# Kernel optimization log

Hardware: AMD Instinct MI355X
Metric: run time of the kernel (lower is better)

## Reference

```python
import jax, jax.numpy as jnp
import numpy as np

WS = 4        # window_size
HEADS = 4     # num_heads
DIM = 128

def _rel_pos_idx(ws):
    # (ws*ws, ws*ws) int index into (2*ws-1)^2 bias table, as in Swin
    coords = np.stack(np.meshgrid(np.arange(ws), np.arange(ws), indexing='ij'))  # (2,ws,ws)
    cf = coords.reshape(2, -1)                       # (2, n)
    rel = cf[:, :, None] - cf[:, None, :]            # (2, n, n)
    rel = rel.transpose(1, 2, 0).astype(np.int64)    # (n, n, 2)
    rel[:, :, 0] += ws - 1
    rel[:, :, 1] += ws - 1
    rel[:, :, 0] *= 2 * ws - 1
    return jnp.asarray(rel.sum(-1))                  # (n, n)

def setup_inputs() -> dict:
    key = jax.random.key(0)
    ks = jax.random.split(key, 6)
    B, H, W, C = 16, 128, 128, DIM
    return {
        "x": jax.random.normal(ks[0], (B, H * W, C), dtype=jnp.float32),
        "H": H,
        "W": W,
        "qkv_w": jax.random.normal(ks[1], (C, 3 * C), dtype=jnp.float32) * 0.02,
        "qkv_b": jax.random.normal(ks[2], (3 * C,), dtype=jnp.float32) * 0.02,
        "proj_w": jax.random.normal(ks[3], (C, C), dtype=jnp.float32) * 0.02,
        "proj_b": jax.random.normal(ks[4], (C,), dtype=jnp.float32) * 0.02,
        "bias_tbl": jax.random.normal(ks[5], ((2 * WS - 1) ** 2, HEADS), dtype=jnp.float32) * 0.02,
    }

def reference(x, H, W, qkv_w, qkv_b, proj_w, proj_b, bias_tbl):
    B, N, C = x.shape
    hd = C // HEADS
    scale = hd ** -0.5
    n = WS * WS
    Hn, Wn = H // WS, W // WS
    # window partition: (B,N,C) -> (B*nW, ws*ws, C)
    xw = x.reshape(B, Hn, WS, Wn, WS, C).transpose(0, 1, 3, 2, 4, 5).reshape(-1, n, C)
    nW = xw.shape[0]
    qkv = xw @ qkv_w + qkv_b                               # (nW, n, 3C)
    qkv = qkv.reshape(nW, n, 3, HEADS, hd).transpose(2, 0, 3, 1, 4)
    q, k, v = qkv[0], qkv[1], qkv[2]                       # (nW, heads, n, hd)
    attn = jnp.einsum('whnd,whmd->whnm', q, k) * scale     # (nW, heads, n, n)
    idx = _rel_pos_idx(WS)
    bias = bias_tbl[idx.reshape(-1)].reshape(n, n, HEADS).transpose(2, 0, 1)  # (heads,n,n)
    attn = jax.nn.softmax(attn + bias[None], axis=-1)
    out = jnp.einsum('whnm,whmd->whnd', attn, v)           # (nW, heads, n, hd)
    out = out.transpose(0, 2, 1, 3).reshape(nW, n, C)
    out = out @ proj_w + proj_b
    # window reverse: (B*nW, n, C) -> (B, N, C)
    out = out.reshape(B, Hn, Wn, WS, WS, C).transpose(0, 1, 3, 2, 4, 5).reshape(B, N, C)
    return out
```

## Files before the change

kernel.cpp:

```cpp
#include <hip/hip_runtime.h>

typedef unsigned short u16;
typedef unsigned int   u32;
typedef __attribute__((ext_vector_type(8))) short bf16x8;
typedef __attribute__((ext_vector_type(4))) short bf16x4;
typedef __attribute__((ext_vector_type(4))) float f32x4;
typedef __attribute__((ext_vector_type(2))) u32 u32x2;

union F8 { bf16x8 v; u32 u[4]; };
union F4 { bf16x4 v; u32 u[2]; };

__device__ __forceinline__ u16 f2b(float f) {
    unsigned u = __builtin_bit_cast(unsigned, f);
    return (u16)((u + 0x7FFFu + ((u >> 16) & 1u)) >> 16);
}
__device__ __forceinline__ u32 pkbf(float a, float b) {
    return ((u32)f2b(b) << 16) | (u32)f2b(a);
}

__device__ __forceinline__ f32x4 mfma16(F4 a, F4 b, f32x4 c) {
    F8 a8, b8;
    a8.u[0] = a.u[0]; a8.u[1] = a.u[1]; a8.u[2] = 0; a8.u[3] = 0;
    b8.u[0] = b.u[0]; b8.u[1] = b.u[1]; b8.u[2] = 0; b8.u[3] = 0;
    return __builtin_amdgcn_mfma_f32_16x16x32_bf16(a8.v, b8.v, c, 0, 0, 0);
}

__device__ __forceinline__ void stage_tile(const u16* wfrag, u16* ldsbase,
                                           int t, int wave, int lane) {
    const char* gp = (const char*)wfrag + (((t * 4 + wave) << 10) | (lane << 4));
    char* lp = (char*)ldsbase + (((t % 3) << 12) | (wave << 10));
    __builtin_amdgcn_global_load_lds(
        (const __attribute__((address_space(1))) void*)gp,
        (__attribute__((address_space(3))) void*)lp, 16, 0, 0);
}

#define PIPE_WAIT(N) { asm volatile("s_waitcnt vmcnt(" #N ")" ::: "memory"); \
    __builtin_amdgcn_sched_barrier(0); __builtin_amdgcn_s_barrier(); }

__global__ void prep_kernel(const float* __restrict__ qkv_w,
                            const float* __restrict__ proj_w,
                            const float* __restrict__ bias_tbl,
                            const float* __restrict__ qkv_b,
                            u16* __restrict__ wsb, float* __restrict__ wsf)
{
    const float scale = 0.17677669529663689f;
    int tid = blockIdx.x * 256 + threadIdx.x;
    if (tid < 49152) {
        int i = tid & 7, l = (tid >> 3) & 63, w = (tid >> 9) & 3, t = tid >> 11;
        int nt;
        if (t < 16) { int h = t >> 2, r = t & 3;
                      nt = (r < 2) ? (2 * h + r) : (8 + 2 * h + (r - 2)); }
        else nt = t;
        int k = w * 32 + (l >> 4) * 8 + i;
        int col = nt * 16 + (l & 15);
        float wv = qkv_w[k * 384 + col];
        if (col < 128) wv *= scale;
        wsb[tid] = f2b(wv);
    } else if (tid < 57344) {
        int e = tid - 49152;
        int nt = e >> 10, rem = e & 1023;
        int c = rem >> 7, le = rem & 127, l = le >> 1, j = le & 1;
        int col = nt * 16 + (l & 15);
        int d = c * 16 + 4 * (l >> 4) + 2 * j;
        u32 val = ((u32)f2b(proj_w[(d + 1) * 128 + col]) << 16)
                |  (u32)f2b(proj_w[d * 128 + col]);
        ((u32*)wsb)[(24 + nt) * 1024 + c * 128 + l * 2 + j] = val;
    } else if (tid < 58368) {
        int e = tid - 57344;
        int h = e >> 8, t1 = (e >> 4) & 15, t2 = e & 15;
        int idx = ((t1 >> 2) - (t2 >> 2) + 3) * 7 + ((t1 & 3) - (t2 & 3) + 3);
        wsf[32768 + e] = bias_tbl[idx * 4 + h];
    } else if (tid < 58752) {
        int e = tid - 58368;
        wsf[33792 + e] = qkv_b[e] * (e < 128 ? scale : 1.0f);
    }
}

__global__ __launch_bounds__(256, 4) void winattn_kernel(
    const float* __restrict__ x, const u16* __restrict__ wfrag,
    const float* __restrict__ proj_b, float* __restrict__ out)
{
    __shared__ alignas(16) u16 lds[11776];
    u16* ring = lds;
    float* qkvbL  = (float*)(lds + 8704);
    float* biasL  = (float*)(lds + 9472);
    float* projbL = (float*)(lds + 11520);

    const int tid  = threadIdx.x;
    const int wave = tid >> 6, lane = tid & 63;
    const int g = lane >> 4, q16 = lane & 15;
    u16* scrA = lds + 6144 + wave * 640;
    u16* scrB = scrA + 320;

    const float* wsf = (const float*)wfrag;
    for (int e = tid; e < 384;  e += 256) qkvbL[e] = wsf[33792 + e];
    for (int e = tid; e < 1024; e += 256) biasL[e] = wsf[32768 + e];
    if (tid < 128) projbL[tid] = proj_b[tid];

    const int wpair = blockIdx.x * 4 + wave;
    const int wid0  = wpair * 2;
    const int b = wid0 >> 10, rem = wid0 & 1023, wi = rem >> 5, wj = rem & 31;
    const int nTok = (wi * 4 + (q16 >> 2)) * 128 + wj * 4 + (q16 & 3);
    const float* xrowA = x + ((long)b * 16384 + nTok) * 128;
    const float* xrowB = xrowA + 512;

    F8 axA[4], axB[4];
    #pragma unroll
    for (int ks = 0; ks < 4; ++ks) {
        const float4* pA = (const float4*)(xrowA + ks * 32 + g * 8);
        float4 a0 = pA[0], a1 = pA[1];
        axA[ks].u[0] = pkbf(a0.x, a0.y); axA[ks].u[1] = pkbf(a0.z, a0.w);
        axA[ks].u[2] = pkbf(a1.x, a1.y); axA[ks].u[3] = pkbf(a1.z, a1.w);
        const float4* pB = (const float4*)(xrowB + ks * 32 + g * 8);
        float4 b0 = pB[0], b1 = pB[1];
        axB[ks].u[0] = pkbf(b0.x, b0.y); axB[ks].u[1] = pkbf(b0.z, b0.w);
        axB[ks].u[2] = pkbf(b1.x, b1.y); axB[ks].u[3] = pkbf(b1.z, b1.w);
    }
    __builtin_amdgcn_sched_barrier(0);
    __syncthreads();

    stage_tile(wfrag, lds, 0, wave, lane);
    stage_tile(wfrag, lds, 1, wave, lane);

    f32x4 z4 = {0.f, 0.f, 0.f, 0.f};
    F4 ones; ones.u[0] = 0x3f803f80u; ones.u[1] = 0x3f803f80u;
    F4 pPA[4], pPB[4];
    float rsA4[4], rsB4[4];
    u32 OpkA[8][2], OpkB[8][2];

    #pragma unroll
    for (int h = 0; h < 4; ++h) {
        u32 QA[2][2], QB[2][2], KA[2][2], KB[2][2];
        #pragma unroll
        for (int r = 0; r < 4; ++r) {
            int t = 4 * h + r;
            PIPE_WAIT(1);
            const u16* slot = ring + (t % 3) * 2048;
            int nt = (r < 2) ? (2 * h + r) : (8 + 2 * h + (r - 2));
            float4 bb = *(const float4*)&qkvbL[nt * 16 + 4 * g];
            f32x4 accA = {bb.x, bb.y, bb.z, bb.w}, accB = accA;
            #pragma unroll
            for (int ks = 0; ks < 4; ++ks) {
                bf16x8 frag = *(const bf16x8*)(slot + ks * 512 + lane * 8);
                accA = __builtin_amdgcn_mfma_f32_16x16x32_bf16(frag, axA[ks].v, accA, 0, 0, 0);
                accB = __builtin_amdgcn_mfma_f32_16x16x32_bf16(frag, axB[ks].v, accB, 0, 0, 0);
            }
            u32 a0 = pkbf(accA[0], accA[1]), a1 = pkbf(accA[2], accA[3]);
            u32 b0 = pkbf(accB[0], accB[1]), b1 = pkbf(accB[2], accB[3]);
            if (r < 2) { QA[r][0] = a0; QA[r][1] = a1; QB[r][0] = b0; QB[r][1] = b1; }
            else { KA[r-2][0] = a0; KA[r-2][1] = a1; KB[r-2][0] = b0; KB[r-2][1] = b1; }
            stage_tile(wfrag, lds, t + 2, wave, lane);
        }
        F8 kfA, qfA, kfB, qfB;
        kfA.u[0]=KA[0][0]; kfA.u[1]=KA[0][1]; kfA.u[2]=KA[1][0]; kfA.u[3]=KA[1][1];
        qfA.u[0]=QA[0][0]; qfA.u[1]=QA[0][1]; qfA.u[2]=QA[1][0]; qfA.u[3]=QA[1][1];
        kfB.u[0]=KB[0][0]; kfB.u[1]=KB[0][1]; kfB.u[2]=KB[1][0]; kfB.u[3]=KB[1][1];
        qfB.u[0]=QB[0][0]; qfB.u[1]=QB[0][1]; qfB.u[2]=QB[1][0]; qfB.u[3]=QB[1][1];
        f32x4 sA = __builtin_amdgcn_mfma_f32_16x16x32_bf16(kfA.v, qfA.v, z4, 0, 0, 0);
        f32x4 sB = __builtin_amdgcn_mfma_f32_16x16x32_bf16(kfB.v, qfB.v, z4, 0, 0, 0);

        float4 bias4 = *(const float4*)&biasL[(h * 16 + q16) * 16 + 4 * g];
        float eA0 = __expf(sA[0] + bias4.x), eA1 = __expf(sA[1] + bias4.y);
        float eA2 = __expf(sA[2] + bias4.z), eA3 = __expf(sA[3] + bias4.w);
        float eB0 = __expf(sB[0] + bias4.x), eB1 = __expf(sB[1] + bias4.y);
        float eB2 = __expf(sB[2] + bias4.z), eB3 = __expf(sB[3] + bias4.w);
        pPA[h].u[0] = pkbf(eA0, eA1); pPA[h].u[1] = pkbf(eA2, eA3);
        pPB[h].u[0] = pkbf(eB0, eB1); pPB[h].u[1] = pkbf(eB2, eB3);
        f32x4 suA = mfma16(ones, pPA[h], z4);
        f32x4 suB = mfma16(ones, pPB[h], z4);
        rsA4[h] = 1.0f / suA[0];
        rsB4[h] = 1.0f / suB[0];
    }

    #pragma unroll
    for (int c = 0; c < 8; ++c) {
        int t = 16 + c;
        PIPE_WAIT(1);
        const u16* slot = ring + (t % 3) * 2048;
        float4 bb = *(const float4*)&qkvbL[(16 + c) * 16 + 4 * g];
        f32x4 accA = {bb.x, bb.y, bb.z, bb.w}, accB = accA;
        #pragma unroll
        for (int ks = 0; ks < 4; ++ks) {
            bf16x8 frag = *(const bf16x8*)(slot + ks * 512 + lane * 8);
            accA = __builtin_amdgcn_mfma_f32_16x16x32_bf16(frag, axA[ks].v, accA, 0, 0, 0);
            accB = __builtin_amdgcn_mfma_f32_16x16x32_bf16(frag, axB[ks].v, accB, 0, 0, 0);
        }
        #pragma unroll
        for (int r = 0; r < 4; ++r) {
            scrA[(4 * g + r) * 20 + q16] = f2b(accA[r]);
            scrB[(4 * g + r) * 20 + q16] = f2b(accB[r]);
        }
        asm volatile("s_waitcnt lgkmcnt(0)" ::: "memory");
        __builtin_amdgcn_sched_barrier(0);
        F4 vfA = *(const F4*)&scrA[q16 * 20 + 4 * g];
        F4 vfB = *(const F4*)&scrB[q16 * 20 + 4 * g];
        int hh = c >> 1;
        f32x4 oA = mfma16(vfA, pPA[hh], z4);
        f32x4 oB = mfma16(vfB, pPB[hh], z4);
        float ra = rsA4[hh], rb = rsB4[hh];
        OpkA[c][0] = pkbf(oA[0] * ra, oA[1] * ra);
        OpkA[c][1] = pkbf(oA[2] * ra, oA[3] * ra);
        OpkB[c][0] = pkbf(oB[0] * rb, oB[1] * rb);
        OpkB[c][1] = pkbf(oB[2] * rb, oB[3] * rb);
        stage_tile(wfrag, lds, t + 2, wave, lane);
    }

    const long obaseA = ((long)b * 16384 + nTok) * 128;
    const long obaseB = obaseA + 512;
    #pragma unroll
    for (int nt = 0; nt < 8; ++nt) {
        int t = 24 + nt;
        if (nt == 0)      PIPE_WAIT(1)
        else if (nt == 7) PIPE_WAIT(2)
        else              PIPE_WAIT(3)
        const u32* slot32 = (const u32*)(ring + (t % 3) * 2048);
        float4 pb = *(const float4*)&projbL[nt * 16 + 4 * g];
        f32x4 accA = {pb.x, pb.y, pb.z, pb.w}, accB = accA;
        #pragma unroll
        for (int cp = 0; cp < 4; ++cp) {
            int c = 2 * cp;
            u32x2 wa = *(const u32x2*)&slot32[c * 128 + lane * 2];
            u32x2 wb = *(const u32x2*)&slot32[(c + 1) * 128 + lane * 2];
            F8 wf; wf.u[0] = wa.x; wf.u[1] = wa.y; wf.u[2] = wb.x; wf.u[3] = wb.y;
            F8 bA; bA.u[0] = OpkA[c][0]; bA.u[1] = OpkA[c][1];
                   bA.u[2] = OpkA[c+1][0]; bA.u[3] = OpkA[c+1][1];
            F8 bB; bB.u[0] = OpkB[c][0]; bB.u[1] = OpkB[c][1];
                   bB.u[2] = OpkB[c+1][0]; bB.u[3] = OpkB[c+1][1];
            accA = __builtin_amdgcn_mfma_f32_16x16x32_bf16(wf.v, bA.v, accA, 0, 0, 0);
            accB = __builtin_amdgcn_mfma_f32_16x16x32_bf16(wf.v, bB.v, accB, 0, 0, 0);
        }
        float4 oA; oA.x = accA[0]; oA.y = accA[1]; oA.z = accA[2]; oA.w = accA[3];
        *(float4*)&out[obaseA + nt * 16 + 4 * g] = oA;
        float4 oB; oB.x = accB[0]; oB.y = accB[1]; oB.z = accB[2]; oB.w = accB[3];
        *(float4*)&out[obaseB + nt * 16 + 4 * g] = oB;
        if (nt < 6) stage_tile(wfrag, lds, t + 2, wave, lane);
    }
}

extern "C" void kernel_launch(void* const* d_in, const int* in_sizes, int n_in,
                              void* d_out, int out_size, void* d_ws, size_t ws_size,
                              hipStream_t stream)
{
    const float* x        = (const float*)d_in[0];
    const float* qkv_w    = (const float*)d_in[3];
    const float* qkv_b    = (const float*)d_in[4];
    const float* proj_w   = (const float*)d_in[5];
    const float* proj_b   = (const float*)d_in[6];
    const float* bias_tbl = (const float*)d_in[7];

    u16*   wsb = (u16*)d_ws;
    float* wsf = (float*)d_ws;

    prep_kernel<<<230, 256, 0, stream>>>(qkv_w, proj_w, bias_tbl, qkv_b, wsb, wsf);
    winattn_kernel<<<2048, 256, 0, stream>>>(x, wsb, proj_b, (float*)d_out);
}
```

Baseline: 75.01 us.

## Stage weight tiles in pairs with a six-slot LDS ring

Moves the weight-tile ring from 3 slots to 6 and issues global-to-LDS loads two tiles at a time, so each pipeline wait plus block barrier now covers two tiles instead of one. The aim is to halve the number of s_waitcnt/barrier synchronisations per block and keep more loads in flight. In exchange LDS use per block grows from about 23 KB to 35 KB, which may limit occupancy at 4 blocks per CU. The vmcnt thresholds are retuned to match the deeper prefetch.

Measured after the change: 75.83 us. No clear change (+1.1%).

```diff
diff --git a/kernel.cpp b/kernel.cpp
--- a/kernel.cpp
+++ b/kernel.cpp
@@ -28,10 +28,15 @@
 __device__ __forceinline__ void stage_tile(const u16* wfrag, u16* ldsbase,
                                            int t, int wave, int lane) {
     const char* gp = (const char*)wfrag + (((t * 4 + wave) << 10) | (lane << 4));
-    char* lp = (char*)ldsbase + (((t % 3) << 12) | (wave << 10));
+    char* lp = (char*)ldsbase + (((t % 6) << 12) | (wave << 10));
     __builtin_amdgcn_global_load_lds(
         (const __attribute__((address_space(1))) void*)gp,
         (__attribute__((address_space(3))) void*)lp, 16, 0, 0);
+}
+__device__ __forceinline__ void stage_phase(const u16* wfrag, u16* ldsbase,
+                                            int p, int wave, int lane) {
+    stage_tile(wfrag, ldsbase, 2 * p,     wave, lane);
+    stage_tile(wfrag, ldsbase, 2 * p + 1, wave, lane);
 }
 
 #define PIPE_WAIT(N) { asm volatile("s_waitcnt vmcnt(" #N ")" ::: "memory"); \
@@ -80,16 +85,16 @@
     const float* __restrict__ x, const u16* __restrict__ wfrag,
     const float* __restrict__ proj_b, float* __restrict__ out)
 {
-    __shared__ alignas(16) u16 lds[11776];
+    __shared__ alignas(16) u16 lds[17920];
     u16* ring = lds;
-    float* qkvbL  = (float*)(lds + 8704);
-    float* biasL  = (float*)(lds + 9472);
-    float* projbL = (float*)(lds + 11520);
+    float* qkvbL  = (float*)(lds + 14848);
+    float* biasL  = (float*)(lds + 15616);
+    float* projbL = (float*)(lds + 17664);
 
     const int tid  = threadIdx.x;
     const int wave = tid >> 6, lane = tid & 63;
     const int g = lane >> 4, q16 = lane & 15;
-    u16* scrA = lds + 6144 + wave * 640;
+    u16* scrA = lds + 12288 + wave * 640;
     u16* scrB = scrA + 320;
 
     const float* wsf = (const float*)wfrag;
@@ -119,8 +124,8 @@
     __builtin_amdgcn_sched_barrier(0);
     __syncthreads();
 
-    stage_tile(wfrag, lds, 0, wave, lane);
-    stage_tile(wfrag, lds, 1, wave, lane);
+    stage_phase(wfrag, lds, 0, wave, lane);
+    stage_phase(wfrag, lds, 1, wave, lane);
 
     f32x4 z4 = {0.f, 0.f, 0.f, 0.f};
     F4 ones; ones.u[0] = 0x3f803f80u; ones.u[1] = 0x3f803f80u;
@@ -128,29 +133,31 @@
     float rsA4[4], rsB4[4];
     u32 OpkA[8][2], OpkB[8][2];
 
+    #define QKV_TILE(T, NT, P0A, P1A, P0B, P1B) {                              \
+        const u16* slot = ring + ((T) % 6) * 2048;                             \
+        float4 bb = *(const float4*)&qkvbL[(NT) * 16 + 4 * g];                 \
+        f32x4 accA = {bb.x, bb.y, bb.z, bb.w}, accB = accA;                    \
+        _Pragma("unroll")                                                      \
+        for (int ks = 0; ks < 4; ++ks) {                                       \
+            bf16x8 frag = *(const bf16x8*)(slot + ks * 512 + lane * 8);        \
+            accA = __builtin_amdgcn_mfma_f32_16x16x32_bf16(frag, axA[ks].v, accA, 0, 0, 0); \
+            accB = __builtin_amdgcn_mfma_f32_16x16x32_bf16(frag, axB[ks].v, accB, 0, 0, 0); \
+        }                                                                      \
+        P0A = pkbf(accA[0], accA[1]); P1A = pkbf(accA[2], accA[3]);            \
+        P0B = pkbf(accB[0], accB[1]); P1B = pkbf(accB[2], accB[3]);            \
+    }
+
     #pragma unroll
     for (int h = 0; h < 4; ++h) {
         u32 QA[2][2], QB[2][2], KA[2][2], KB[2][2];
-        #pragma unroll
-        for (int r = 0; r < 4; ++r) {
-            int t = 4 * h + r;
-            PIPE_WAIT(1);
-            const u16* slot = ring + (t % 3) * 2048;
-            int nt = (r < 2) ? (2 * h + r) : (8 + 2 * h + (r - 2));
-            float4 bb = *(const float4*)&qkvbL[nt * 16 + 4 * g];
-            f32x4 accA = {bb.x, bb.y, bb.z, bb.w}, accB = accA;
-            #pragma unroll
-            for (int ks = 0; ks < 4; ++ks) {
-                bf16x8 frag = *(const bf16x8*)(slot + ks * 512 + lane * 8);
-                accA = __builtin_amdgcn_mfma_f32_16x16x32_bf16(frag, axA[ks].v, accA, 0, 0, 0);
-                accB = __builtin_amdgcn_mfma_f32_16x16x32_bf16(frag, axB[ks].v, accB, 0, 0, 0);
-            }
-            u32 a0 = pkbf(accA[0], accA[1]), a1 = pkbf(accA[2], accA[3]);
-            u32 b0 = pkbf(accB[0], accB[1]), b1 = pkbf(accB[2], accB[3]);
-            if (r < 2) { QA[r][0] = a0; QA[r][1] = a1; QB[r][0] = b0; QB[r][1] = b1; }
-            else { KA[r-2][0] = a0; KA[r-2][1] = a1; KB[r-2][0] = b0; KB[r-2][1] = b1; }
-            stage_tile(wfrag, lds, t + 2, wave, lane);
-        }
+        PIPE_WAIT(2);
+        QKV_TILE(4*h,     2*h,     QA[0][0], QA[0][1], QB[0][0], QB[0][1]);
+        QKV_TILE(4*h + 1, 2*h + 1, QA[1][0], QA[1][1], QB[1][0], QB[1][1]);
+        stage_phase(wfrag, lds, 2*h + 2, wave, lane);
+        PIPE_WAIT(2);
+        QKV_TILE(4*h + 2, 8 + 2*h, KA[0][0], KA[0][1], KB[0][0], KB[0][1]);
+        QKV_TILE(4*h + 3, 9 + 2*h, KA[1][0], KA[1][1], KB[1][0], KB[1][1]);
+        stage_phase(wfrag, lds, 2*h + 3, wave, lane);
         F8 kfA, qfA, kfB, qfB;
         kfA.u[0]=KA[0][0]; kfA.u[1]=KA[0][1]; kfA.u[2]=KA[1][0]; kfA.u[3]=KA[1][1];
         qfA.u[0]=QA[0][0]; qfA.u[1]=QA[0][1]; qfA.u[2]=QA[1][0]; qfA.u[3]=QA[1][1];
@@ -158,7 +165,6 @@
         qfB.u[0]=QB[0][0]; qfB.u[1]=QB[0][1]; qfB.u[2]=QB[1][0]; qfB.u[3]=QB[1][1];
         f32x4 sA = __builtin_amdgcn_mfma_f32_16x16x32_bf16(kfA.v, qfA.v, z4, 0, 0, 0);
         f32x4 sB = __builtin_amdgcn_mfma_f32_16x16x32_bf16(kfB.v, qfB.v, z4, 0, 0, 0);
-
         float4 bias4 = *(const float4*)&biasL[(h * 16 + q16) * 16 + 4 * g];
         float eA0 = __expf(sA[0] + bias4.x), eA1 = __expf(sA[1] + bias4.y);
         float eA2 = __expf(sA[2] + bias4.z), eA3 = __expf(sA[3] + bias4.w);
@@ -173,67 +179,72 @@
     }
 
     #pragma unroll
-    for (int c = 0; c < 8; ++c) {
-        int t = 16 + c;
-        PIPE_WAIT(1);
-        const u16* slot = ring + (t % 3) * 2048;
-        float4 bb = *(const float4*)&qkvbL[(16 + c) * 16 + 4 * g];
-        f32x4 accA = {bb.x, bb.y, bb.z, bb.w}, accB = accA;
+    for (int f = 0; f < 4; ++f) {
+        PIPE_WAIT(2);
         #pragma unroll
-        for (int ks = 0; ks < 4; ++ks) {
-            bf16x8 frag = *(const bf16x8*)(slot + ks * 512 + lane * 8);
-            accA = __builtin_amdgcn_mfma_f32_16x16x32_bf16(frag, axA[ks].v, accA, 0, 0, 0);
-            accB = __builtin_amdgcn_mfma_f32_16x16x32_bf16(frag, axB[ks].v, accB, 0, 0, 0);
+        for (int s = 0; s < 2; ++s) {
+            int c = 2 * f + s;
+            const u16* slot = ring + ((16 + c) % 6) * 2048;
+            float4 bb = *(const float4*)&qkvbL[(16 + c) * 16 + 4 * g];
+            f32x4 accA = {bb.x, bb.y, bb.z, bb.w}, accB = accA;
+            #pragma unroll
+            for (int ks = 0; ks < 4; ++ks) {
+                bf16x8 frag = *(const bf16x8*)(slot + ks * 512 + lane * 8);
+                accA = __builtin_amdgcn_mfma_f32_16x16x32_bf16(frag, axA[ks].v, accA, 0, 0, 0);
+                accB = __builtin_amdgcn_mfma_f32_16x16x32_bf16(frag, axB[ks].v, accB, 0, 0, 0);
+            }
+            #pragma unroll
+            for (int r = 0; r < 4; ++r) {
+                scrA[(4 * g + r) * 20 + q16] = f2b(accA[r]);
+                scrB[(4 * g + r) * 20 + q16] = f2b(accB[r]);
+            }
+            asm volatile("s_waitcnt lgkmcnt(0)" ::: "memory");
+            __builtin_amdgcn_sched_barrier(0);
+            F4 vfA = *(const F4*)&scrA[q16 * 20 + 4 * g];
+            F4 vfB = *(const F4*)&scrB[q16 * 20 + 4 * g];
+            f32x4 oA = mfma16(vfA, pPA[f], z4);
+            f32x4 oB = mfma16(vfB, pPB[f], z4);
+            float ra = rsA4[f], rb = rsB4[f];
+            OpkA[c][0] = pkbf(oA[0] * ra, oA[1] * ra);
+            OpkA[c][1] = pkbf(oA[2] * ra, oA[3] * ra);
+            OpkB[c][0] = pkbf(oB[0] * rb, oB[1] * rb);
+            OpkB[c][1] = pkbf(oB[2] * rb, oB[3] * rb);
         }
-        #pragma unroll
-        for (int r = 0; r < 4; ++r) {
-            scrA[(4 * g + r) * 20 + q16] = f2b(accA[r]);
-            scrB[(4 * g + r) * 20 + q16] = f2b(accB[r]);
-        }
-        asm volatile("s_waitcnt lgkmcnt(0)" ::: "memory");
-        __builtin_amdgcn_sched_barrier(0);
-        F4 vfA = *(const F4*)&scrA[q16 * 20 + 4 * g];
-        F4 vfB = *(const F4*)&scrB[q16 * 20 + 4 * g];
-        int hh = c >> 1;
-        f32x4 oA = mfma16(vfA, pPA[hh], z4);
-        f32x4 oB = mfma16(vfB, pPB[hh], z4);
-        float ra = rsA4[hh], rb = rsB4[hh];
-        OpkA[c][0] = pkbf(oA[0] * ra, oA[1] * ra);
-        OpkA[c][1] = pkbf(oA[2] * ra, oA[3] * ra);
-        OpkB[c][0] = pkbf(oB[0] * rb, oB[1] * rb);
-        OpkB[c][1] = pkbf(oB[2] * rb, oB[3] * rb);
-        stage_tile(wfrag, lds, t + 2, wave, lane);
+        stage_phase(wfrag, lds, 10 + f, wave, lane);
     }
 
     const long obaseA = ((long)b * 16384 + nTok) * 128;
     const long obaseB = obaseA + 512;
     #pragma unroll
-    for (int nt = 0; nt < 8; ++nt) {
-        int t = 24 + nt;
-        if (nt == 0)      PIPE_WAIT(1)
-        else if (nt == 7) PIPE_WAIT(2)
-        else              PIPE_WAIT(3)
-        const u32* slot32 = (const u32*)(ring + (t % 3) * 2048);
-        float4 pb = *(const float4*)&projbL[nt * 16 + 4 * g];
-        f32x4 accA = {pb.x, pb.y, pb.z, pb.w}, accB = accA;
+    for (int f = 0; f < 4; ++f) {
+        if (f == 0)      PIPE_WAIT(2)
+        else if (f == 3) PIPE_WAIT(4)
+        else             PIPE_WAIT(6)
         #pragma unroll
-        for (int cp = 0; cp < 4; ++cp) {
-            int c = 2 * cp;
-            u32x2 wa = *(const u32x2*)&slot32[c * 128 + lane * 2];
-            u32x2 wb = *(const u32x2*)&slot32[(c + 1) * 128 + lane * 2];
-            F8 wf; wf.u[0] = wa.x; wf.u[1] = wa.y; wf.u[2] = wb.x; wf.u[3] = wb.y;
-            F8 bA; bA.u[0] = OpkA[c][0]; bA.u[1] = OpkA[c][1];
-                   bA.u[2] = OpkA[c+1][0]; bA.u[3] = OpkA[c+1][1];
-            F8 bB; bB.u[0] = OpkB[c][0]; bB.u[1] = OpkB[c][1];
-                   bB.u[2] = OpkB[c+1][0]; bB.u[3] = OpkB[c+1][1];
-            accA = __builtin_amdgcn_mfma_f32_16x16x32_bf16(wf.v, bA.v, accA, 0, 0, 0);
-            accB = __builtin_amdgcn_mfma_f32_16x16x32_bf16(wf.v, bB.v, accB, 0, 0, 0);
+        for (int s = 0; s < 2; ++s) {
+            int nt = 2 * f + s;
+            const u32* slot32 = (const u32*)(ring + ((24 + nt) % 6) * 2048);
+            float4 pb = *(const float4*)&projbL[nt * 16 + 4 * g];
+            f32x4 accA = {pb.x, pb.y, pb.z, pb.w}, accB = accA;
+            #pragma unroll
+            for (int cp = 0; cp < 4; ++cp) {
+                int c = 2 * cp;
+                u32x2 wa = *(const u32x2*)&slot32[c * 128 + lane * 2];
+                u32x2 wb = *(const u32x2*)&slot32[(c + 1) * 128 + lane * 2];
+                F8 wf; wf.u[0] = wa.x; wf.u[1] = wa.y; wf.u[2] = wb.x; wf.u[3] = wb.y;
+                F8 bA; bA.u[0] = OpkA[c][0]; bA.u[1] = OpkA[c][1];
+                       bA.u[2] = OpkA[c+1][0]; bA.u[3] = OpkA[c+1][1];
+                F8 bB; bB.u[0] = OpkB[c][0]; bB.u[1] = OpkB[c][1];
+                       bB.u[2] = OpkB[c+1][0]; bB.u[3] = OpkB[c+1][1];
+                accA = __builtin_amdgcn_mfma_f32_16x16x32_bf16(wf.v, bA.v, accA, 0, 0, 0);
+                accB = __builtin_amdgcn_mfma_f32_16x16x32_bf16(wf.v, bB.v, accB, 0, 0, 0);
+            }
+            float4 oA; oA.x = accA[0]; oA.y = accA[1]; oA.z = accA[2]; oA.w = accA[3];
+            *(float4*)&out[obaseA + nt * 16 + 4 * g] = oA;
+            float4 oB; oB.x = accB[0]; oB.y = accB[1]; oB.z = accB[2]; oB.w = accB[3];
+            *(float4*)&out[obaseB + nt * 16 + 4 * g] = oB;
         }
-        float4 oA; oA.x = accA[0]; oA.y = accA[1]; oA.z = accA[2]; oA.w = accA[3];
-        *(float4*)&out[obaseA + nt * 16 + 4 * g] = oA;
-        float4 oB; oB.x = accB[0]; oB.y = accB[1]; oB.z = accB[2]; oB.w = accB[3];
-        *(float4*)&out[obaseB + nt * 16 + 4 * g] = oB;
-        if (nt < 6) stage_tile(wfrag, lds, t + 2, wave, lane);
+        if (f < 2) stage_phase(wfrag, lds, 14 + f, wave, lane);
     }
 }
 
```
